# Optimization experiments

Measured on AMD Instinct MI355X. Metric: run time of the kernel, lower is better.

The kernel has to match this reference:

```python
import jax, jax.numpy as jnp
import numpy as np

EPS = 0.1

def setup_inputs() -> dict:
    key = jax.random.key(0)
    k1, k2, k3, k4, k5, k6 = jax.random.split(key, 6)
    B, N, Cin, Cout = 8, 2048, 128, 128
    x = jax.random.normal(k1, (B, N, Cin), dtype=jnp.float32)
    x_0 = jax.random.normal(k2, (B, N, Cout), dtype=jnp.float32)
    adj = jax.random.randint(k3, (B, N, N), 0, 2, dtype=jnp.int32)
    # learned parameters (Linear without bias stores weight [out,in]; we keep [in,out])
    W_lin = jax.random.normal(k4, (Cin, Cout), dtype=jnp.float32) / np.sqrt(Cin)
    w_att_l = jax.random.normal(k5, (Cout,), dtype=jnp.float32) / np.sqrt(Cout)
    w_att_r = jax.random.normal(k6, (Cout,), dtype=jnp.float32) / np.sqrt(Cout)
    return {"x": x, "x_0": x_0, "adj": adj, "W_lin": W_lin, "w_att_l": w_att_l, "w_att_r": w_att_r}

def reference(x, x_0, adj, W_lin, w_att_l, w_att_r):
    # x: [B,N,Cin] -> h: [B,N,Cout]
    h = jnp.einsum('bni,io->bno', x, W_lin)
    alpha_l = jnp.einsum('bno,o->bn', h, w_att_l)  # [B,N]
    alpha_r = jnp.einsum('bno,o->bn', h, w_att_r)  # [B,N]
    # alpha[b,i,j] = tanh(alpha_r[b,i] * alpha_l[b,j])
    alpha = jnp.tanh(alpha_r[:, :, None] * alpha_l[:, None, :])  # [B,N,N]
    alpha = jnp.where(adj == 0, jnp.float32(0.0), alpha)
    # dropout p=0.0 -> identity
    out = jnp.einsum('bij,bjo->bio', alpha, h)  # [B,N,Cout]
    return out + EPS * x_0
```

## Files before the change

kernel.cpp:

```cpp
#include <hip/hip_runtime.h>
#include <stdint.h>

#define B_   8
#define N_   2048
#define C_   128
#define EPS_ 0.1f

typedef __attribute__((ext_vector_type(8))) short short8;
typedef __attribute__((ext_vector_type(4))) float f32x4;

__device__ __forceinline__ unsigned short f2bf(float f) {
    union { float f; uint32_t u; } v; v.f = f;
    uint32_t u = v.u + 0x7FFF + ((v.u >> 16) & 1);
    return (unsigned short)(u >> 16);
}

__global__ __launch_bounds__(128) void k_wt(const float* __restrict__ W,
                                            unsigned short* __restrict__ Wt) {
    const int o = blockIdx.x, k = threadIdx.x;
    Wt[o * C_ + k] = f2bf(W[k * C_ + o]);
}

__global__ __launch_bounds__(256) void k_h(
    const float* __restrict__ x, const unsigned short* __restrict__ Wt,
    const float* __restrict__ wl, const float* __restrict__ wr,
    unsigned short* __restrict__ ht, float* __restrict__ al, float* __restrict__ ar)
{
    const int b    = blockIdx.x >> 5;
    const int i0   = (blockIdx.x & 31) * 64;
    const int t    = threadIdx.x;
    const int lane = t & 63;
    const int wid  = t >> 6;

    __shared__ __align__(16) unsigned short xs[64 * 128];
    __shared__ __align__(16) unsigned short ws[128 * 128];

    #pragma unroll
    for (int p = 0; p < 4; ++p) {
        const int s = p * 256 + t, row = s >> 4, u = s & 15;
        const float* gp = x + ((size_t)(b * N_ + i0 + row) * C_ + u * 8);
        float4 f0 = *(const float4*)gp;
        float4 f1 = *(const float4*)(gp + 4);
        short8 tv;
        tv[0] = (short)f2bf(f0.x); tv[1] = (short)f2bf(f0.y);
        tv[2] = (short)f2bf(f0.z); tv[3] = (short)f2bf(f0.w);
        tv[4] = (short)f2bf(f1.x); tv[5] = (short)f2bf(f1.y);
        tv[6] = (short)f2bf(f1.z); tv[7] = (short)f2bf(f1.w);
        *(short8*)&xs[row * 128 + (u ^ (row & 15)) * 8] = tv;
    }
    #pragma unroll
    for (int p = 0; p < 8; ++p) {
        const int s = p * 256 + t, o = s >> 4, u = s & 15;
        int4 v = *(const int4*)(Wt + o * C_ + u * 8);
        *(int4*)&ws[o * 128 + (u ^ (o & 15)) * 8] = v;
    }
    __syncthreads();

    const int m0 = wid * 16, lr = lane & 15, q = lane >> 4;
    f32x4 acc[8];
    #pragma unroll
    for (int i = 0; i < 8; ++i) acc[i] = (f32x4){0.f, 0.f, 0.f, 0.f};

    #pragma unroll
    for (int s = 0; s < 4; ++s) {
        const int m = m0 + lr;
        short8 af = *(const short8*)&xs[m * 128 + ((s * 4 + q) ^ (m & 15)) * 8];
        #pragma unroll
        for (int tt = 0; tt < 8; ++tt) {
            const int o = tt * 16 + lr;
            short8 bf = *(const short8*)&ws[o * 128 + ((s * 4 + q) ^ (o & 15)) * 8];
            acc[tt] = __builtin_amdgcn_mfma_f32_16x16x32_bf16(af, bf, acc[tt], 0, 0, 0);
        }
    }

    float pl[4] = {0.f, 0.f, 0.f, 0.f}, pr[4] = {0.f, 0.f, 0.f, 0.f};
    const int j0 = i0 + m0 + q * 4;
    #pragma unroll
    for (int tt = 0; tt < 8; ++tt) {
        const int o = tt * 16 + lr;
        const float wlv = wl[o], wrv = wr[o];
        unsigned int lo = (unsigned int)f2bf(acc[tt][0]) | ((unsigned int)f2bf(acc[tt][1]) << 16);
        unsigned int hi = (unsigned int)f2bf(acc[tt][2]) | ((unsigned int)f2bf(acc[tt][3]) << 16);
        uint2 u2; u2.x = lo; u2.y = hi;
        *(uint2*)&ht[((size_t)(b * C_ + o)) * N_ + j0] = u2;
        #pragma unroll
        for (int r = 0; r < 4; ++r) {
            pl[r] = fmaf(acc[tt][r], wlv, pl[r]);
            pr[r] = fmaf(acc[tt][r], wrv, pr[r]);
        }
    }
    #pragma unroll
    for (int msk = 1; msk < 16; msk <<= 1) {
        #pragma unroll
        for (int r = 0; r < 4; ++r) {
            pl[r] += __shfl_xor(pl[r], msk, 64);
            pr[r] += __shfl_xor(pr[r], msk, 64);
        }
    }
    if (lr == 0) {
        #pragma unroll
        for (int r = 0; r < 4; ++r) {
            al[b * N_ + j0 + r] = pl[r];
            ar[b * N_ + j0 + r] = pr[r];
        }
    }
}

struct Pref {
    int4   a0, a1;
    int4   h0, h1, h2, h3;
    float4 l0, l1;
};

__global__ __launch_bounds__(256) void k_out(
    const int* __restrict__ adj, const unsigned short* __restrict__ ht,
    const float* __restrict__ al, const float* __restrict__ ar,
    const float* __restrict__ x0, float* __restrict__ out)
{
    const int b    = blockIdx.x >> 6;
    const int i0   = (blockIdx.x & 63) * 32;
    const int t    = threadIdx.x;
    const int lane = t & 63;
    const int wid  = t >> 6;

    __shared__ __align__(16) unsigned short a_s[2][32 * 64];
    __shared__ __align__(16) unsigned short h_s[2][128 * 64];

    const int arow = t >> 3;
    const int jq   = t & 7;
    const float arv = ar[b * N_ + i0 + arow];

    auto ldc = [&](int c) -> Pref {
        Pref P;
        const int j0 = c * 64;
        const int* ap = adj + ((size_t)(b * N_) + i0 + arow) * N_ + j0 + jq * 8;
        P.a0 = *(const int4*)ap;
        P.a1 = *(const int4*)(ap + 4);
        const unsigned short* hp = ht + (size_t)b * C_ * N_ + j0 + jq * 8;
        P.h0 = *(const int4*)(hp + (size_t)arow * N_);
        P.h1 = *(const int4*)(hp + (size_t)(arow + 32) * N_);
        P.h2 = *(const int4*)(hp + (size_t)(arow + 64) * N_);
        P.h3 = *(const int4*)(hp + (size_t)(arow + 96) * N_);
        const float* alp = al + b * N_ + j0 + jq * 8;
        P.l0 = *(const float4*)alp;
        P.l1 = *(const float4*)(alp + 4);
        return P;
    };

    auto stage = [&](int buf, const Pref& P) {
        short8 pk;
        const int*   av = (const int*)&P.a0;
        const int*   bv = (const int*)&P.a1;
        const float* af = (const float*)&P.l0;
        const float* bf = (const float*)&P.l1;
        #pragma unroll
        for (int e = 0; e < 4; ++e) {
            float z  = arv * af[e];
            float ex = __expf(2.f * z);
            float th = 1.f - 2.f / (ex + 1.f);
            pk[e] = av[e] ? (short)f2bf(th) : (short)0;
        }
        #pragma unroll
        for (int e = 0; e < 4; ++e) {
            float z  = arv * bf[e];
            float ex = __expf(2.f * z);
            float th = 1.f - 2.f / (ex + 1.f);
            pk[4 + e] = bv[e] ? (short)f2bf(th) : (short)0;
        }
        const int su = (jq ^ (arow & 7)) * 8;
        *(short8*)&a_s[buf][arow * 64 + su] = pk;
        *(int4*)&h_s[buf][(arow)      * 64 + su] = P.h0;
        *(int4*)&h_s[buf][(arow + 32) * 64 + su] = P.h1;
        *(int4*)&h_s[buf][(arow + 64) * 64 + su] = P.h2;
        *(int4*)&h_s[buf][(arow + 96) * 64 + su] = P.h3;
    };

    const int m0 = (wid & 1) * 16, n0 = (wid >> 1) * 64;
    const int lr = lane & 15, q = lane >> 4;
    f32x4 acc[4];
    #pragma unroll
    for (int i = 0; i < 4; ++i) acc[i] = (f32x4){0.f, 0.f, 0.f, 0.f};

    auto mma = [&](int buf) {
        #pragma unroll
        for (int s2 = 0; s2 < 2; ++s2) {
            const int m = m0 + lr;
            short8 afr = *(const short8*)&a_s[buf][m * 64 + ((s2 * 4 + q) ^ (m & 7)) * 8];
            #pragma unroll
            for (int tt = 0; tt < 4; ++tt) {
                const int o = n0 + tt * 16 + lr;
                short8 bfr = *(const short8*)&h_s[buf][o * 64 + ((s2 * 4 + q) ^ (o & 7)) * 8];
                acc[tt] = __builtin_amdgcn_mfma_f32_16x16x32_bf16(afr, bfr, acc[tt], 0, 0, 0);
            }
        }
    };

    {
        Pref p = ldc(0);
        stage(0, p);
    }
    Pref pA = ldc(1);
    Pref pB = ldc(2);
    __syncthreads();

    for (int cc = 0; cc < 16; ++cc) {
        stage(1, pA);
        if (cc < 15) pA = ldc(2 * cc + 3);
        mma(0);
        __syncthreads();

        if (cc < 15) {
            stage(0, pB);
            if (cc < 14) pB = ldc(2 * cc + 4);
        }
        mma(1);
        __syncthreads();
    }

    #pragma unroll
    for (int tt = 0; tt < 4; ++tt) {
        const int o = n0 + tt * 16 + lr;
        #pragma unroll
        for (int r = 0; r < 4; ++r) {
            const int row = i0 + m0 + q * 4 + r;
            const size_t idx = ((size_t)(b * N_) + row) * C_ + o;
            out[idx] = acc[tt][r] + EPS_ * x0[idx];
        }
    }
}

extern "C" void kernel_launch(void* const* d_in, const int* in_sizes, int n_in,
                              void* d_out, int out_size, void* d_ws, size_t ws_size,
                              hipStream_t stream) {
    const float* x   = (const float*)d_in[0];
    const float* x0  = (const float*)d_in[1];
    const int*   adj = (const int*)d_in[2];
    const float* W   = (const float*)d_in[3];
    const float* wl  = (const float*)d_in[4];
    const float* wr  = (const float*)d_in[5];
    float* out = (float*)d_out;

    unsigned short* ht = (unsigned short*)d_ws;
    float* al = (float*)((char*)d_ws + (size_t)B_ * C_ * N_ * 2);
    float* ar = al + B_ * N_;
    unsigned short* Wt = (unsigned short*)(ar + B_ * N_);

    k_wt <<<C_,             C_,  0, stream>>>(W, Wt);
    k_h  <<<B_ * (N_ / 64), 256, 0, stream>>>(x, Wt, wl, wr, ht, al, ar);
    k_out<<<B_ * (N_ / 32), 256, 0, stream>>>(adj, ht, al, ar, x0, out);
}
```

Before: 227.4 us.

## Pre-pack int32 adjacency into a bitmask before the aggregation kernel

Adds a streaming kernel that reads the int32 adjacency matrix and uses wave ballots to pack each group of 64 entries into a 64-bit mask. The main aggregation kernel then loads one byte per 8 neighbours instead of two int4 vectors, which shrinks its per-thread register prefetch and its global traffic. The aim is to move the bulky adjacency read into a simple, fully coalesced pass that can run near peak bandwidth. In exchange it adds an extra launch and a small bitmask write and read through workspace memory.

```diff
diff --git a/kernel.cpp b/kernel.cpp
--- a/kernel.cpp
+++ b/kernel.cpp
@@ -19,6 +19,29 @@
                                             unsigned short* __restrict__ Wt) {
     const int o = blockIdx.x, k = threadIdx.x;
     Wt[o * C_ + k] = f2bf(W[k * C_ + o]);
+}
+
+__global__ __launch_bounds__(256) void k_adj(const int* __restrict__ adj,
+                                             unsigned long long* __restrict__ adjm) {
+    const int lane = threadIdx.x & 63;
+    const size_t gw   = ((size_t)blockIdx.x * 256 + threadIdx.x) >> 6;
+    const size_t seg0 = gw * 64;
+    #pragma unroll 1
+    for (int s = 0; s < 64; s += 8) {
+        int v[8];
+        #pragma unroll
+        for (int u = 0; u < 8; ++u)
+            v[u] = adj[(seg0 + s + u) * 64 + lane];
+        unsigned long long m[8];
+        #pragma unroll
+        for (int u = 0; u < 8; ++u)
+            m[u] = __ballot(v[u] != 0);
+        if (lane == 0) {
+            #pragma unroll
+            for (int u = 0; u < 8; ++u)
+                adjm[seg0 + s + u] = m[u];
+        }
+    }
 }
 
 __global__ __launch_bounds__(256) void k_h(
@@ -107,13 +130,13 @@
 }
 
 struct Pref {
-    int4   a0, a1;
+    unsigned int ab;
     int4   h0, h1, h2, h3;
     float4 l0, l1;
 };
 
 __global__ __launch_bounds__(256) void k_out(
-    const int* __restrict__ adj, const unsigned short* __restrict__ ht,
+    const unsigned char* __restrict__ adjm8, const unsigned short* __restrict__ ht,
     const float* __restrict__ al, const float* __restrict__ ar,
     const float* __restrict__ x0, float* __restrict__ out)
 {
@@ -129,13 +152,12 @@
     const int arow = t >> 3;
     const int jq   = t & 7;
     const float arv = ar[b * N_ + i0 + arow];
+    const unsigned char* abase = adjm8 + ((size_t)(b * N_) + i0 + arow) * (N_ / 8) + jq;
 
     auto ldc = [&](int c) -> Pref {
         Pref P;
         const int j0 = c * 64;
-        const int* ap = adj + ((size_t)(b * N_) + i0 + arow) * N_ + j0 + jq * 8;
-        P.a0 = *(const int4*)ap;
-        P.a1 = *(const int4*)(ap + 4);
+        P.ab = abase[c * 8];
         const unsigned short* hp = ht + (size_t)b * C_ * N_ + j0 + jq * 8;
         P.h0 = *(const int4*)(hp + (size_t)arow * N_);
         P.h1 = *(const int4*)(hp + (size_t)(arow + 32) * N_);
@@ -149,8 +171,6 @@
 
     auto stage = [&](int buf, const Pref& P) {
         short8 pk;
-        const int*   av = (const int*)&P.a0;
-        const int*   bv = (const int*)&P.a1;
         const float* af = (const float*)&P.l0;
         const float* bf = (const float*)&P.l1;
         #pragma unroll
@@ -158,14 +178,14 @@
             float z  = arv * af[e];
             float ex = __expf(2.f * z);
             float th = 1.f - 2.f / (ex + 1.f);
-            pk[e] = av[e] ? (short)f2bf(th) : (short)0;
+            pk[e] = (P.ab & (1u << e)) ? (short)f2bf(th) : (short)0;
         }
         #pragma unroll
         for (int e = 0; e < 4; ++e) {
             float z  = arv * bf[e];
             float ex = __expf(2.f * z);
             float th = 1.f - 2.f / (ex + 1.f);
-            pk[4 + e] = bv[e] ? (short)f2bf(th) : (short)0;
+            pk[4 + e] = (P.ab & (1u << (4 + e))) ? (short)f2bf(th) : (short)0;
         }
         const int su = (jq ^ (arow & 7)) * 8;
         *(short8*)&a_s[buf][arow * 64 + su] = pk;
@@ -244,8 +264,10 @@
     float* al = (float*)((char*)d_ws + (size_t)B_ * C_ * N_ * 2);
     float* ar = al + B_ * N_;
     unsigned short* Wt = (unsigned short*)(ar + B_ * N_);
+    unsigned long long* adjm = (unsigned long long*)((char*)Wt + (size_t)C_ * C_ * 2);
 
     k_wt <<<C_,             C_,  0, stream>>>(W, Wt);
+    k_adj<<<2048,           256, 0, stream>>>(adj, adjm);
     k_h  <<<B_ * (N_ / 64), 256, 0, stream>>>(x, Wt, wl, wr, ht, al, ar);
-    k_out<<<B_ * (N_ / 32), 256, 0, stream>>>(adj, ht, al, ar, x0, out);
-}
+    k_out<<<B_ * (N_ / 32), 256, 0, stream>>>((const unsigned char*)adjm, ht, al, ar, x0, out);
+}
```

After: 255.6 us. 1.12x slower.

## Load MFMA operands directly from global into registers, drop LDS staging

Applied to the files above, without the earlier changes.

The output kernel no longer stages adjacency-derived alpha and h tiles through shared memory with barriers. Each lane now loads its own MFMA A/B fragments straight from global memory into registers, computes tanh/mask per lane, and double-buffers in registers. This removes LDS writes/reads and __syncthreads, but each wave recomputes tanh for rows shared with other waves and loads h redundantly (the two M-waves load the same h), increasing global/L2 traffic and register pressure.

```diff
diff --git a/kernel.cpp b/kernel.cpp
--- a/kernel.cpp
+++ b/kernel.cpp
@@ -107,9 +107,9 @@
 }
 
 struct Pref {
-    int4   a0, a1;
-    int4   h0, h1, h2, h3;
-    float4 l0, l1;
+    int4   a[4];
+    float4 l[4];
+    int4   hb[8];
 };
 
 __global__ __launch_bounds__(256) void k_out(
@@ -123,98 +123,65 @@
     const int lane = t & 63;
     const int wid  = t >> 6;
 
-    __shared__ __align__(16) unsigned short a_s[2][32 * 64];
-    __shared__ __align__(16) unsigned short h_s[2][128 * 64];
-
-    const int arow = t >> 3;
-    const int jq   = t & 7;
-    const float arv = ar[b * N_ + i0 + arow];
+    const int m0 = (wid & 1) * 16, n0 = (wid >> 1) * 64;
+    const int lr = lane & 15, q = lane >> 4;
+    const int q8 = q * 8;
+
+    const int irow = i0 + m0 + lr;
+    const float arv = ar[b * N_ + irow];
+    const float tl  = 2.f * arv;
+    const int*            adjp = adj + ((size_t)(b * N_) + irow) * N_;
+    const float*          alp  = al + b * N_;
+    const unsigned short* hbp  = ht + ((size_t)(b * C_) + n0 + lr) * N_;
 
     auto ldc = [&](int c) -> Pref {
         Pref P;
-        const int j0 = c * 64;
-        const int* ap = adj + ((size_t)(b * N_) + i0 + arow) * N_ + j0 + jq * 8;
-        P.a0 = *(const int4*)ap;
-        P.a1 = *(const int4*)(ap + 4);
-        const unsigned short* hp = ht + (size_t)b * C_ * N_ + j0 + jq * 8;
-        P.h0 = *(const int4*)(hp + (size_t)arow * N_);
-        P.h1 = *(const int4*)(hp + (size_t)(arow + 32) * N_);
-        P.h2 = *(const int4*)(hp + (size_t)(arow + 64) * N_);
-        P.h3 = *(const int4*)(hp + (size_t)(arow + 96) * N_);
-        const float* alp = al + b * N_ + j0 + jq * 8;
-        P.l0 = *(const float4*)alp;
-        P.l1 = *(const float4*)(alp + 4);
+        const int j0 = c * 64 + q8;
+        #pragma unroll
+        for (int s2 = 0; s2 < 2; ++s2) {
+            P.a[s2 * 2]     = *(const int4*)(adjp + j0 + s2 * 32);
+            P.a[s2 * 2 + 1] = *(const int4*)(adjp + j0 + s2 * 32 + 4);
+            P.l[s2 * 2]     = *(const float4*)(alp + j0 + s2 * 32);
+            P.l[s2 * 2 + 1] = *(const float4*)(alp + j0 + s2 * 32 + 4);
+            #pragma unroll
+            for (int tt = 0; tt < 4; ++tt)
+                P.hb[s2 * 4 + tt] =
+                    *(const int4*)(hbp + (size_t)(tt * 16) * N_ + j0 + s2 * 32);
+        }
         return P;
     };
 
-    auto stage = [&](int buf, const Pref& P) {
-        short8 pk;
-        const int*   av = (const int*)&P.a0;
-        const int*   bv = (const int*)&P.a1;
-        const float* af = (const float*)&P.l0;
-        const float* bf = (const float*)&P.l1;
-        #pragma unroll
-        for (int e = 0; e < 4; ++e) {
-            float z  = arv * af[e];
-            float ex = __expf(2.f * z);
-            float th = 1.f - 2.f / (ex + 1.f);
-            pk[e] = av[e] ? (short)f2bf(th) : (short)0;
-        }
-        #pragma unroll
-        for (int e = 0; e < 4; ++e) {
-            float z  = arv * bf[e];
-            float ex = __expf(2.f * z);
-            float th = 1.f - 2.f / (ex + 1.f);
-            pk[4 + e] = bv[e] ? (short)f2bf(th) : (short)0;
-        }
-        const int su = (jq ^ (arow & 7)) * 8;
-        *(short8*)&a_s[buf][arow * 64 + su] = pk;
-        *(int4*)&h_s[buf][(arow)      * 64 + su] = P.h0;
-        *(int4*)&h_s[buf][(arow + 32) * 64 + su] = P.h1;
-        *(int4*)&h_s[buf][(arow + 64) * 64 + su] = P.h2;
-        *(int4*)&h_s[buf][(arow + 96) * 64 + su] = P.h3;
-    };
-
-    const int m0 = (wid & 1) * 16, n0 = (wid >> 1) * 64;
-    const int lr = lane & 15, q = lane >> 4;
     f32x4 acc[4];
     #pragma unroll
     for (int i = 0; i < 4; ++i) acc[i] = (f32x4){0.f, 0.f, 0.f, 0.f};
 
-    auto mma = [&](int buf) {
+    auto cmp = [&](const Pref& P) {
         #pragma unroll
         for (int s2 = 0; s2 < 2; ++s2) {
-            const int m = m0 + lr;
-            short8 afr = *(const short8*)&a_s[buf][m * 64 + ((s2 * 4 + q) ^ (m & 7)) * 8];
+            const int*   av = (const int*)&P.a[s2 * 2];
+            const float* lv = (const float*)&P.l[s2 * 2];
+            short8 af;
+            #pragma unroll
+            for (int e = 0; e < 8; ++e) {
+                float ex = __expf(tl * lv[e]);
+                float th = 1.f - 2.f / (ex + 1.f);
+                af[e] = av[e] ? (short)f2bf(th) : (short)0;
+            }
             #pragma unroll
             for (int tt = 0; tt < 4; ++tt) {
-                const int o = n0 + tt * 16 + lr;
-                short8 bfr = *(const short8*)&h_s[buf][o * 64 + ((s2 * 4 + q) ^ (o & 7)) * 8];
-                acc[tt] = __builtin_amdgcn_mfma_f32_16x16x32_bf16(afr, bfr, acc[tt], 0, 0, 0);
+                short8 bf = *(const short8*)&P.hb[s2 * 4 + tt];
+                acc[tt] = __builtin_amdgcn_mfma_f32_16x16x32_bf16(af, bf, acc[tt], 0, 0, 0);
             }
         }
     };
 
-    {
-        Pref p = ldc(0);
-        stage(0, p);
-    }
-    Pref pA = ldc(1);
-    Pref pB = ldc(2);
-    __syncthreads();
-
-    for (int cc = 0; cc < 16; ++cc) {
-        stage(1, pA);
-        if (cc < 15) pA = ldc(2 * cc + 3);
-        mma(0);
-        __syncthreads();
-
-        if (cc < 15) {
-            stage(0, pB);
-            if (cc < 14) pB = ldc(2 * cc + 4);
-        }
-        mma(1);
-        __syncthreads();
+    Pref PA = ldc(0);
+    #pragma unroll 1
+    for (int c = 0; c < 32; c += 2) {
+        Pref PB = ldc(c + 1);
+        cmp(PA);
+        if (c + 2 < 32) PA = ldc(c + 2);
+        cmp(PB);
     }
 
     #pragma unroll
```

After: 270.3 us. +18.9%, slower.
